# Optimization experiments

Hardware: AMD Instinct MI355X
Metric: run time of the kernel (lower is better)

## Reference

```python
import jax, jax.numpy as jnp
import numpy as np

SR = 16000
FRAME = 400      # int(0.025*SR)
HOP = 160        # int(0.01*SR)
MINP, MAXP = 32, 320   # SR/500, SR/50
NFFT_FRAME = 1024      # next pow2 >= 2*FRAME-1
NFFT_FULL = 262144     # >= samples + max hnr lag (160000+200)
LN_EPS = 1e-5


def _frame(a):
    n = a.shape[0]
    nf = (n - FRAME - 1) // HOP + 1  # len(range(0, n-FRAME, HOP))
    idx = jnp.arange(nf)[:, None] * HOP + jnp.arange(FRAME)[None, :]
    return a[idx]  # [nf, FRAME]


def _autocorr(x, nfft, nlags):
    # linear autocorrelation via FFT; nfft >= len + nlags avoids circular wrap
    X = jnp.fft.rfft(x, n=nfft)
    ac = jnp.fft.irfft(X * jnp.conj(X), n=nfft)
    return ac[..., :nlags]


def _masked_mean_std(x, m):
    cnt = m.sum()
    c = jnp.maximum(cnt, 1.0)
    mean = jnp.sum(x * m) / c
    var = jnp.sum(((x - mean) ** 2) * m) / c
    return jnp.where(cnt > 0, mean, 0.0), jnp.where(cnt > 0, jnp.sqrt(var), 0.0)


def _compact(vals, mask, fill_len):
    # pack masked values to the front (stable); first k=sum(mask) entries valid
    rank = jnp.cumsum(mask) - 1
    idx = jnp.where(mask, rank, fill_len)
    return jnp.zeros(fill_len, vals.dtype).at[idx].set(vals, mode='drop')


def _prosody_single(a):
    n = a.shape[0]
    frames = _frame(a)
    nf = frames.shape[0]
    # --- energy ---
    rms = jnp.sqrt(jnp.mean(frames ** 2, axis=-1))
    e_mean, e_std = rms.mean(), rms.std()
    # --- zero-crossing rate ---
    zcr = jnp.sum(jnp.abs(jnp.diff(jnp.sign(frames), axis=-1)), axis=-1) / (2.0 * FRAME)
    z_mean, z_std = zcr.mean(), zcr.std()
    # --- F0 via per-frame autocorrelation peak picking ---
    ac = _autocorr(frames, NFFT_FRAME, MAXP)            # [nf, 320]
    peak = jnp.argmax(ac[:, MINP:MAXP], axis=-1) + MINP  # first max, like np.argmax
    ac_pk = jnp.take_along_axis(ac, peak[:, None], axis=-1)[:, 0]
    f0 = SR / peak.astype(jnp.float32)
    valid = (ac_pk > 0.3 * ac[:, 0]) & (f0 > 50.0) & (f0 < 500.0)
    f0_mean, f0_std = _masked_mean_std(f0, valid.astype(jnp.float32))
    # --- jitter: rising threshold crossings over the whole waveform ---
    thr = 0.3 * jnp.max(jnp.abs(a))
    cross = (a[:-1] < thr) & (a[1:] >= thr)  # crossing at index i in [1, n)
    pos = jnp.arange(1, n)
    k = cross.sum()
    posarr = _compact(pos, cross, n)
    periods = (posarr[1:] - posarr[:-1]).astype(jnp.float32)
    nper = k - 1
    pmask = jnp.arange(n - 1) < nper
    mean_period = jnp.sum(periods * pmask) / jnp.maximum(nper, 1)
    pdiffs = jnp.abs(periods[1:] - periods[:-1])
    dmask = jnp.arange(n - 2) < (nper - 1)
    mean_pdiff = jnp.sum(pdiffs * dmask) / jnp.maximum(nper - 1, 1)
    jitter = jnp.where((nper >= 2) & (mean_period > 0),
                       jnp.clip(mean_pdiff / jnp.maximum(mean_period, 1e-12), 0.0, 1.0), 0.0)
    jitter = jnp.where((f0_mean < 50.0) | (f0_mean > 500.0), 0.0, jitter)
    # --- shimmer: diffs of consecutive retained (>0.01) frame peak amps ---
    amp = jnp.max(jnp.abs(frames), axis=-1)
    amask = amp > 0.01
    ka = amask.sum()
    amparr = _compact(amp, amask, nf)
    adiffs = jnp.abs(amparr[1:] - amparr[:-1])
    admask = jnp.arange(nf - 1) < (ka - 1)
    mean_amp = jnp.sum(amparr * (jnp.arange(nf) < ka)) / jnp.maximum(ka, 1)
    mean_adiff = jnp.sum(adiffs * admask) / jnp.maximum(ka - 1, 1)
    shimmer = jnp.where((ka >= 2) & (mean_amp > 0),
                        jnp.clip(mean_adiff / jnp.maximum(mean_amp, 1e-12), 0.0, 1.0), 0.0)
    # --- HNR: full-signal autocorrelation, lags 50..199 ---
    seg = _autocorr(a, NFFT_FULL, 200)[50:200]
    sig_peak = jnp.max(seg)
    noise_floor = jnp.percentile(seg, 10.0)  # numpy-default linear interpolation
    hnr = jnp.where(noise_floor > 0,
                    jnp.clip(sig_peak / jnp.maximum(noise_floor, 1e-30) / 100.0, 0.0, 1.0), 0.0)
    # --- voicing rate (energy + zcr thresholds; source truncated, see notes) ---
    voiced = (rms > 0.01) & (zcr < 0.3)
    voicing_rate = voiced.mean()
    feats = jnp.stack([f0_mean / 500.0, f0_std / 100.0, e_mean, e_std,
                       z_mean, z_std, jitter, shimmer, hnr, voicing_rate])
    metrics = jnp.stack([f0_mean, f0_std, e_mean, e_std, z_mean, z_std,
                         jitter, shimmer, hnr, voicing_rate])
    return feats, metrics


def _project(feats, W1, b1, gamma, beta, W2, b2):
    h = feats @ W1.T + b1
    mu = h.mean(-1, keepdims=True)
    var = h.var(-1, keepdims=True)
    h = (h - mu) / jnp.sqrt(var + LN_EPS) * gamma + beta
    h = jax.nn.relu(h)          # dropout = identity (eval mode)
    return h @ W2.T + b2


def setup_inputs() -> dict:
    key = jax.random.key(0)
    ks = jax.random.split(key, 7)
    B, N = 128, 160000
    return {
        'raw_audio': jax.random.normal(ks[0], (B, N), dtype=jnp.float32) * 0.5,
        'W1': jax.random.normal(ks[1], (64, 10), dtype=jnp.float32) * 0.3,
        'b1': jax.random.normal(ks[2], (64,), dtype=jnp.float32) * 0.01,
        'gamma': jnp.ones((64,), dtype=jnp.float32),
        'beta': jnp.zeros((64,), dtype=jnp.float32),
        'W2': jax.random.normal(ks[3], (128, 64), dtype=jnp.float32) * 0.1,
        'b2': jax.random.normal(ks[4], (128,), dtype=jnp.float32) * 0.01,
    }


def reference(raw_audio, W1, b1, gamma, beta, W2, b2):
    feats, metrics = jax.vmap(_prosody_single)(raw_audio)  # [B,10], [B,10]
    feats = jax.lax.stop_gradient(feats)  # torch detaches via numpy round-trip
    proj = _project(feats, W1, b1, gamma, beta, W2, b2)    # [B,128]
    return proj, metrics
```

## Files before the change

kernel.cpp:

```cpp
#include <hip/hip_runtime.h>
#include <stdint.h>

typedef unsigned int uint;
typedef unsigned short ushort;
typedef unsigned long long ull;
typedef __attribute__((ext_vector_type(8))) short bf16x8;
typedef __attribute__((ext_vector_type(4))) float f32x4;

#define SR_F 16000.0f
#define NSAMP 160000
#define NB 128
#define FRAME 400
#define HOP 160
#define NF 998
#define NHNR_CHUNK 10
#define JCH 125
#define HNR_LAGS 150
#define TJ 25
#define HWIN (32*TJ + 304)
#define NJB 10
#define TAIL0 ((NF - 1) * HOP + FRAME)

#define HXO 562
#define HREG 1116

#define OFF_RMS 0
#define OFF_ZCR (OFF_RMS + NB*NF)
#define OFF_AMP (OFF_ZCR + NB*NF)
#define OFF_F0  (OFF_AMP + NB*NF)
#define OFF_VAL (OFF_F0  + NB*NF)
#define OFF_HNR (OFF_VAL + NB*NF)
#define OFF_JST (OFF_HNR + NB*NHNR_CHUNK*HNR_LAGS)

__device__ __forceinline__ int imax_(int a, int b) { return a > b ? a : b; }
__device__ __forceinline__ int imin2_(int a, int b) { return a < b ? a : b; }

__device__ __forceinline__ int   f2i(float v) { return __builtin_bit_cast(int, v); }
__device__ __forceinline__ float i2f(int v)   { return __builtin_bit_cast(float, v); }
__device__ __forceinline__ uint  f2u(float v) { return __builtin_bit_cast(uint, v); }

#if __has_builtin(__builtin_amdgcn_permlane16_swap) && __has_builtin(__builtin_amdgcn_permlane32_swap)
#define HAVE_PLSWAP 1
#endif

template<int C>
__device__ __forceinline__ int dpp_i(int x) {
    return __builtin_amdgcn_update_dpp(0, x, C, 0xf, 0xf, true);
}
template<int C>
__device__ __forceinline__ float dpp_f(float x) { return i2f(dpp_i<C>(f2i(x))); }

__device__ __forceinline__ float wred_sum(float x) {
#ifdef HAVE_PLSWAP
    x += dpp_f<0xB1>(x);
    x += dpp_f<0x4E>(x);
    x += dpp_f<0x141>(x);
    x += dpp_f<0x140>(x);
    {
        auto r = __builtin_amdgcn_permlane16_swap(f2i(x), f2i(x), false, false);
        x = i2f((int)r[0]) + i2f((int)r[1]);
    }
    {
        auto r = __builtin_amdgcn_permlane32_swap(f2i(x), f2i(x), false, false);
        x = i2f((int)r[0]) + i2f((int)r[1]);
    }
#else
    #pragma unroll
    for (int off = 32; off; off >>= 1) x += __shfl_xor(x, off);
#endif
    return x;
}

__device__ __forceinline__ float wred_max(float x) {
#ifdef HAVE_PLSWAP
    x = fmaxf(x, dpp_f<0xB1>(x));
    x = fmaxf(x, dpp_f<0x4E>(x));
    x = fmaxf(x, dpp_f<0x141>(x));
    x = fmaxf(x, dpp_f<0x140>(x));
    {
        auto r = __builtin_amdgcn_permlane16_swap(f2i(x), f2i(x), false, false);
        x = fmaxf(i2f((int)r[0]), i2f((int)r[1]));
    }
    {
        auto r = __builtin_amdgcn_permlane32_swap(f2i(x), f2i(x), false, false);
        x = fmaxf(i2f((int)r[0]), i2f((int)r[1]));
    }
#else
    #pragma unroll
    for (int off = 32; off; off >>= 1) x = fmaxf(x, __shfl_xor(x, off));
#endif
    return x;
}

__device__ __forceinline__ int wred_imin(int x) {
#ifdef HAVE_PLSWAP
    x = imin2_(x, dpp_i<0xB1>(x));
    x = imin2_(x, dpp_i<0x4E>(x));
    x = imin2_(x, dpp_i<0x141>(x));
    x = imin2_(x, dpp_i<0x140>(x));
    {
        auto r = __builtin_amdgcn_permlane16_swap(x, x, false, false);
        x = imin2_((int)r[0], (int)r[1]);
    }
    {
        auto r = __builtin_amdgcn_permlane32_swap(x, x, false, false);
        x = imin2_((int)r[0], (int)r[1]);
    }
#else
    #pragma unroll
    for (int off = 32; off; off >>= 1) x = imin2_(x, __shfl_xor(x, off));
#endif
    return x;
}

__device__ __forceinline__ uint cvtpk_bf16(float a, float b) {
    uint r;
    asm("v_cvt_pk_bf16_f32 %0, %1, %2" : "=v"(r) : "v"(a), "v"(b));
    return r;
}

__device__ __forceinline__ bf16x8 ld_b_frag(const uint* p) {
    union { uint u[4]; bf16x8 v; } t;
    t.u[0] = p[0]; t.u[1] = p[1]; t.u[2] = p[2]; t.u[3] = p[3];
    return t.v;
}

__device__ __forceinline__ int sx_(float a, float b) {
    return (int)((f2u(a) ^ f2u(b)) >> 31);
}

struct JSt { int cnt, p0, p1, pl, pl2; float sum; };

__device__ __forceinline__ void jmerge(JSt& A, const JSt& r) {
    if (r.cnt == 0) return;
    if (A.cnt == 0) { A = r; return; }
    int pb = r.p0 - A.pl;
    A.sum += r.sum;
    if (A.cnt >= 2) A.sum += fabsf((float)(pb - (A.pl - A.pl2)));
    if (r.cnt >= 2) A.sum += fabsf((float)((r.p1 - r.p0) - pb));
    if (A.cnt == 1) A.p1 = r.p0;
    A.pl2 = (r.cnt >= 2) ? r.pl2 : A.pl;
    A.pl = r.pl;
    A.cnt += r.cnt;
}

__device__ __forceinline__ JSt jword(unsigned long long word, int wb) {
    JSt st; st.cnt = 0; st.p0 = 0; st.p1 = 0; st.pl = 0; st.pl2 = 0; st.sum = 0.f;
    while (word) {
        int b = __builtin_ctzll(word);
        word &= word - 1;
        int pos = wb + b + 1;
        if (st.cnt >= 2) st.sum += fabsf((float)((pos - st.pl) - (st.pl - st.pl2)));
        if (st.cnt == 0) st.p0 = pos;
        if (st.cnt == 1) st.p1 = pos;
        st.pl2 = st.pl; st.pl = pos; ++st.cnt;
    }
    return st;
}

__global__ __launch_bounds__(256) void k_frame(const float* __restrict__ audio,
                                               float* __restrict__ ws)
{
    __shared__ __align__(16) uint lds[4][744];
    const int tid = threadIdx.x;
    const int widx = tid >> 6, lane = tid & 63;
    const int lo = lane & 15, q = lane >> 4;
    const int s = blockIdx.y;
    const int fbase = blockIdx.x * 16 + widx * 4;
    const float* as = audio + (size_t)s * NSAMP;

    uint* base = lds[widx];
    ull* zb = (ull*)base;
    const ushort* xw_us = (const ushort*)base;

    for (int i = lane; i < 168; i += 64) {
        int zi;
        if (i < 60)       zi = i;
        else if (i < 84)  zi = 160 + (i - 60);
        else if (i < 144) zi = 185 + (i - 84);
        else              zi = 345 + (i - 144);
        zb[zi] = 0ull;
    }

    float4 tA, tB; float bnA, bnB;
    {
        int f0 = fbase; if (f0 > NF - 1) f0 = NF - 1;
        const float* a = as + (size_t)f0 * HOP;
        tA  = ((const float4*)a)[lane];
        bnA = a[4 * lane + 4];
        tB.x = tB.y = tB.z = tB.w = 0.f; bnB = 0.f;
        if (lane < 36) {
            tB  = ((const float4*)a)[64 + lane];
            bnB = (lane < 35) ? a[4 * (64 + lane) + 4] : 0.f;
        }
    }

    for (int p = 0; p < 4; ++p) {
        int f = fbase + p; if (f > NF - 1) f = NF - 1;

        float amp; int zci;
        {
            amp = fmaxf(fmaxf(fabsf(tA.x), fabsf(tA.y)),
                        fmaxf(fabsf(tA.z), fabsf(tA.w)));
            zci = sx_(tA.x, tA.y) + sx_(tA.y, tA.z)
                + sx_(tA.z, tA.w) + sx_(tA.w, bnA);
            ull w = (ull)cvtpk_bf16(tA.x, tA.y) | ((ull)cvtpk_bf16(tA.z, tA.w) << 32);
            ull o = (ull)cvtpk_bf16(tA.y, tA.z) | ((ull)cvtpk_bf16(tA.w, bnA) << 32);
            zb[60 + lane]  = w;
            zb[245 + lane] = o;
        }
        if (lane < 36) {
            amp = fmaxf(amp, fmaxf(fmaxf(fabsf(tB.x), fabsf(tB.y)),
                                   fmaxf(fabsf(tB.z), fabsf(tB.w))));
            zci += sx_(tB.x, tB.y) + sx_(tB.y, tB.z) + sx_(tB.z, tB.w);
            if (lane < 35) zci += sx_(tB.w, bnB);
            ull w = (ull)cvtpk_bf16(tB.x, tB.y) | ((ull)cvtpk_bf16(tB.z, tB.w) << 32);
            ull o = (ull)cvtpk_bf16(tB.y, tB.z) | ((ull)cvtpk_bf16(tB.w, bnB) << 32);
            zb[124 + lane] = w;
            zb[309 + lane] = o;
        }
        float zcs = wred_sum((float)zci);
        amp = wred_max(amp);

        __syncthreads();

        float4 nA, nB; float nbA = 0.f, nbB = 0.f;
        nA.x = nA.y = nA.z = nA.w = 0.f; nB = nA;
        if (p < 3) {
            int fn = fbase + p + 1; if (fn > NF - 1) fn = NF - 1;
            const float* an = as + (size_t)fn * HOP;
            nA  = ((const float4*)an)[lane];
            nbA = an[4 * lane + 4];
            if (lane < 36) {
                nB  = ((const float4*)an)[64 + lane];
                nbB = (lane < 35) ? an[4 * (64 + lane) + 4] : 0.f;
            }
        }

        f32x4 acc1 = {0.f, 0.f, 0.f, 0.f};
        f32x4 acc2 = {0.f, 0.f, 0.f, 0.f};
        const int a_eb = 240 + 8 * q - 16 * lo;
        const uint* bp = base + ((lo & 1) ? 370 : 0) + 120 + 4 * q + (lo >> 1);
        bf16x8 ah[5];

        #pragma unroll
        for (int j = 0; j < 13; ++j) {
            bf16x8 a1 = *(const bf16x8*)(xw_us + a_eb + 32 * j);
            bf16x8 b  = ld_b_frag(bp + 16 * j);
            acc1 = __builtin_amdgcn_mfma_f32_16x16x32_bf16(a1, b, acc1, 0, 0, 0);
            if (j < 5) ah[j] = a1;
            if (j >= 8)
                acc2 = __builtin_amdgcn_mfma_f32_16x16x32_bf16(ah[j - 8], b, acc2, 0, 0, 0);
        }

        float ac0 = i2f(__builtin_amdgcn_readfirstlane(f2i(acc1[0])));

        float bv = -1e30f; int bl = 1 << 30;
        #pragma unroll
        for (int r = 0; r < 4; ++r) {
            int lag = 64 * q + 16 * r + lo;
            float v = acc1[r];
            if (lag >= 32 && v > bv) { bv = v; bl = lag; }
        }
        if (q == 0) {
            #pragma unroll
            for (int r = 0; r < 4; ++r) {
                int lag = 256 + 16 * r + lo;
                float v = acc2[r];
                if (v > bv) { bv = v; bl = lag; }
            }
        }
        float mv = wred_max(bv);
        int   ml = wred_imin((bv == mv) ? bl : (1 << 30));

        if (lane == 0) {
            float f0v = SR_F / (float)ml;
            int valid = (mv > 0.3f * ac0) && (f0v > 50.f) && (f0v < 500.f);
            size_t idx = (size_t)s * NF + f;
            ws[OFF_RMS + idx] = sqrtf(fmaxf(ac0, 0.f) / (float)FRAME);
            ws[OFF_ZCR + idx] = zcs / 400.f;
            ws[OFF_AMP + idx] = amp;
            ws[OFF_F0  + idx] = f0v;
            ws[OFF_VAL + idx] = valid ? 1.f : 0.f;
        }

        tA = nA; tB = nB; bnA = nbA; bnB = nbB;
        __syncthreads();
    }
}

__global__ __launch_bounds__(256) void k_hnr(const float* __restrict__ audio,
                                             float* __restrict__ ws)
{
    __shared__ __align__(16) uint hxd[4][HREG];
    __shared__ unsigned long long msk[250];
    __shared__ __align__(16) uint pool[1504];
    __shared__ JSt sg[25];
    __shared__ float swmax[4];
    const int tid = threadIdx.x;
    const int widx = tid >> 6, lane = tid & 63;
    const int lo = lane & 15, q = lane >> 4;
    const int s = blockIdx.y;
    const int c = blockIdx.x * 4 + widx;
    const float* a = audio + (size_t)s * NSAMP;

    float (*hred)[152] = (float (*)[152])pool;
    JSt* sw = (JSt*)pool;

    uint* xwd = hxd[widx];
    uint* xod = hxd[widx] + HXO;
    const ushort* xw = (const ushort*)xwd;

    const int aoff = 240 + 8 * q - 16 * lo;
    const uint* bw = (lo & 1) ? xod : xwd;
    const int boff = 144 + 4 * q + (lo >> 1);

    f32x4 acc = {0.f, 0.f, 0.f, 0.f};

    for (int tile = 0; tile < JCH / TJ; ++tile) {
        const int g0 = 32 * (c * JCH + tile * TJ) - 288;
        for (int v = lane; v < HWIN / 4; v += 64) {
            int g = g0 + 4 * v;
            float x0, x1, x2, x3, x4;
            if (g >= 0 && g + 4 < NSAMP) {
                float4 t = *(const float4*)(a + g);
                x0 = t.x; x1 = t.y; x2 = t.z; x3 = t.w;
                x4 = a[g + 4];
            } else {
                x0 = (g     >= 0 && g     < NSAMP) ? a[g]     : 0.f;
                x1 = (g + 1 >= 0 && g + 1 < NSAMP) ? a[g + 1] : 0.f;
                x2 = (g + 2 >= 0 && g + 2 < NSAMP) ? a[g + 2] : 0.f;
                x3 = (g + 3 >= 0 && g + 3 < NSAMP) ? a[g + 3] : 0.f;
                x4 = (g + 4 >= 0 && g + 4 < NSAMP) ? a[g + 4] : 0.f;
            }
            int d = 2 * v;
            xwd[d] = cvtpk_bf16(x0, x1); xwd[d + 1] = cvtpk_bf16(x2, x3);
            xod[d] = cvtpk_bf16(x1, x2); xod[d + 1] = cvtpk_bf16(x3, x4);
        }
        asm volatile("" ::: "memory");
        __builtin_amdgcn_sched_barrier(0);

        #pragma unroll
        for (int jl = 0; jl < TJ; ++jl) {
            bf16x8 af = *(const bf16x8*)(xw + aoff + 32 * jl);
            bf16x8 bf = ld_b_frag(bw + boff + 16 * jl);
            acc = __builtin_amdgcn_mfma_f32_16x16x32_bf16(af, bf, acc, 0, 0, 0);
        }
        asm volatile("" ::: "memory");
        __builtin_amdgcn_sched_barrier(0);
    }

    #pragma unroll
    for (int r = 0; r < 4; ++r) {
        int row = 4 * q + r;
        int lag = 48 + 16 * row + lo;
        if (row < 10 && lag >= 50 && lag < 200)
            hred[widx][lag - 50] = acc[r];
    }
    __syncthreads();
    if (tid < HNR_LAGS) {
        float v = hred[0][tid] + hred[1][tid] + hred[2][tid] + hred[3][tid];
        ws[OFF_HNR + ((size_t)s * NHNR_CHUNK + blockIdx.x) * HNR_LAGS + tid] = v;
    }

    float m = 0.f;
    const float* ampA = ws + OFF_AMP + (size_t)s * NF;
    for (int i = tid; i < NF; i += 256) m = fmaxf(m, ampA[i]);
    if (tid < NSAMP - TAIL0) m = fmaxf(m, fabsf(a[TAIL0 + tid]));
    m = wred_max(m);
    if ((tid & 63) == 0) swmax[tid >> 6] = m;
    __syncthreads();
    const float thr = 0.3f * fmaxf(fmaxf(swmax[0], swmax[1]),
                                   fmaxf(swmax[2], swmax[3]));

    const int cbase = blockIdx.x * 16000;
    for (int ot = 0; ot < 9; ++ot) {
        float va[7], vb[7];
        #pragma unroll
        for (int k = 0; k < 7; ++k) {
            int off = (ot * 7 + k) * 256 + tid;
            int i = cbase + off;
            bool in = (off < 16000) && (i < NSAMP - 1);
            va[k] = in ? a[i] : 1e30f;
            vb[k] = in ? a[i + 1] : 1e30f;
        }
        #pragma unroll
        for (int k = 0; k < 7; ++k) {
            int off = (ot * 7 + k) * 256 + tid;
            bool fl = (va[k] < thr) && (vb[k] >= thr);
            unsigned long long bal = __ballot(fl);
            int w = off >> 6;
            if ((tid & 63) == 0 && w < 250) msk[w] = bal;
        }
    }
    __syncthreads();

    if (tid < 250) sw[tid] = jword(msk[tid], cbase + tid * 64);
    __syncthreads();
    if (tid < 25) {
        JSt A = sw[10 * tid];
        #pragma unroll
        for (int k = 1; k < 10; ++k) jmerge(A, sw[10 * tid + k]);
        sg[tid] = A;
    }
    __syncthreads();
    if (tid == 0) {
        JSt A = sg[0];
        for (int k = 1; k < 25; ++k) jmerge(A, sg[k]);
        float* jp = ws + OFF_JST + ((size_t)s * NJB + blockIdx.x) * 6;
        jp[0] = (float)A.cnt; jp[1] = (float)A.p0; jp[2] = (float)A.p1;
        jp[3] = (float)A.pl;  jp[4] = (float)A.pl2; jp[5] = A.sum;
    }
}

__global__ __launch_bounds__(256) void k_final(const float* __restrict__ ws,
        const float* __restrict__ W1, const float* __restrict__ b1,
        const float* __restrict__ gam, const float* __restrict__ bet,
        const float* __restrict__ W2, const float* __restrict__ b2,
        float* __restrict__ out)
{
    __shared__ float samp[NF];
    __shared__ float sac[HNR_LAGS];
    __shared__ float sred[32];
    __shared__ float sstat[11];
    __shared__ float sjit[4];
    __shared__ float sfeats[10];
    __shared__ float shid[64];
    __shared__ float ssa[250][5];
    __shared__ float ssg[25][5];

    const int s = blockIdx.x;
    const int tid = threadIdx.x;
    const float* rmsA = ws + OFF_RMS + (size_t)s * NF;
    const float* zcrA = ws + OFF_ZCR + (size_t)s * NF;
    const float* ampA = ws + OFF_AMP + (size_t)s * NF;
    const float* f0A  = ws + OFF_F0  + (size_t)s * NF;
    const float* valA = ws + OFF_VAL + (size_t)s * NF;

    float a0=0,a1=0,a2=0,a3=0,a4=0,a5=0,a6=0,a7=0;
    for (int i = tid; i < NF; i += 256) {
        float r = rmsA[i], z = zcrA[i], f0 = f0A[i], v = valA[i];
        samp[i] = ampA[i];
        a0 += r; a1 += r * r; a2 += z; a3 += z * z;
        a4 += f0 * v; a5 += f0 * f0 * v; a6 += v;
        a7 += (r > 0.01f && z < 0.3f) ? 1.f : 0.f;
    }
    #pragma unroll
    for (int off = 32; off; off >>= 1) {
        a0 += __shfl_xor(a0, off); a1 += __shfl_xor(a1, off);
        a2 += __shfl_xor(a2, off); a3 += __shfl_xor(a3, off);
        a4 += __shfl_xor(a4, off); a5 += __shfl_xor(a5, off);
        a6 += __shfl_xor(a6, off); a7 += __shfl_xor(a7, off);
    }
    if ((tid & 63) == 0) {
        int w = tid >> 6;
        sred[w*8+0]=a0; sred[w*8+1]=a1; sred[w*8+2]=a2; sred[w*8+3]=a3;
        sred[w*8+4]=a4; sred[w*8+5]=a5; sred[w*8+6]=a6; sred[w*8+7]=a7;
    }
    __syncthreads();

    if (tid < HNR_LAGS) {
        float acc = 0.f;
        const float* p = ws + OFF_HNR + (size_t)s * NHNR_CHUNK * HNR_LAGS + tid;
        #pragma unroll
        for (int c = 0; c < NHNR_CHUNK; ++c) acc += p[c * HNR_LAGS];
        sac[tid] = acc;
    }
    if (tid == 0) {
        for (int k = 0; k < 8; ++k)
            sstat[k] = sred[k] + sred[8+k] + sred[16+k] + sred[24+k];
    }
    if (tid < 250) {
        int i0 = tid * 4;
        float cnt=0.f, first=0.f, last=0.f, ssum=0.f, sad=0.f;
        #pragma unroll
        for (int k = 0; k < 4; ++k) {
            int i = i0 + k;
            if (i < NF) {
                float av = samp[i];
                if (av > 0.01f) {
                    if (cnt >= 1.f) sad += fabsf(av - last);
                    else first = av;
                    ssum += av; last = av; cnt += 1.f;
                }
            }
        }
        ssa[tid][0]=cnt; ssa[tid][1]=first; ssa[tid][2]=last;
        ssa[tid][3]=ssum; ssa[tid][4]=sad;
    }
    __syncthreads();

    if (tid < HNR_LAGS) {
        float v = sac[tid];
        int r = 0;
        for (int j = 0; j < HNR_LAGS; ++j) {
            float vj = sac[j];
            r += (vj < v) || (vj == v && j < tid);
        }
        if (r == 14) sstat[8] = v;
        if (r == 15) sstat[9] = v;
    }
    if (tid == 160) {
        const float* jp = ws + OFF_JST + (size_t)s * NJB * 6;
        JSt A; A.cnt = 0; A.p0 = 0; A.p1 = 0; A.pl = 0; A.pl2 = 0; A.sum = 0.f;
        for (int c = 0; c < NJB; ++c) {
            JSt r;
            r.cnt = (int)jp[c*6+0]; r.p0 = (int)jp[c*6+1]; r.p1 = (int)jp[c*6+2];
            r.pl  = (int)jp[c*6+3]; r.pl2 = (int)jp[c*6+4]; r.sum = jp[c*6+5];
            jmerge(A, r);
        }
        sjit[0] = (float)A.cnt; sjit[1] = (float)A.p0;
        sjit[2] = (float)A.pl;  sjit[3] = A.sum;
    }
    if (tid == 192) {
        float mx = sac[0];
        for (int j = 1; j < HNR_LAGS; ++j) mx = fmaxf(mx, sac[j]);
        sstat[10] = mx;
    }
    if (tid >= 200 && tid < 225) {
        int t2 = tid - 200;
        float cnt=0.f, first=0.f, last=0.f, ssum=0.f, sad=0.f;
        #pragma unroll
        for (int k = 0; k < 10; ++k) {
            int j = 10 * t2 + k;
            float c2 = ssa[j][0];
            if (c2 > 0.f) {
                if (cnt > 0.f) sad += ssa[j][4] + fabsf(ssa[j][1] - last);
                else { first = ssa[j][1]; sad += ssa[j][4]; }
                ssum += ssa[j][3]; last = ssa[j][2]; cnt += c2;
            }
        }
        ssg[t2][0]=cnt; ssg[t2][1]=first; ssg[t2][2]=last;
        ssg[t2][3]=ssum; ssg[t2][4]=sad;
    }
    __syncthreads();

    if (tid == 0) {
        float S_r = sstat[0], S_r2 = sstat[1], S_z = sstat[2], S_z2 = sstat[3];
        float S_f = sstat[4], S_f2 = sstat[5], S_v = sstat[6], S_voi = sstat[7];
        float e_mean = S_r / (float)NF;
        float e_std  = sqrtf(fmaxf(S_r2 / (float)NF - e_mean * e_mean, 0.f));
        float z_mean = S_z / (float)NF;
        float z_std  = sqrtf(fmaxf(S_z2 / (float)NF - z_mean * z_mean, 0.f));
        float f0_mean = 0.f, f0_std = 0.f;
        if (S_v > 0.f) {
            f0_mean = S_f / S_v;
            f0_std  = sqrtf(fmaxf(S_f2 / S_v - f0_mean * f0_mean, 0.f));
        }
        int k = (int)sjit[0];
        float pp0 = sjit[1], ppl = sjit[2], psum = sjit[3];
        int nper = k - 1;
        float mean_period = (k >= 2) ? (ppl - pp0) / (float)(k - 1) : 0.f;
        float mean_pd = psum / (float)imax_(nper - 1, 1);
        float jit = (nper >= 2 && mean_period > 0.f)
            ? fminf(fmaxf(mean_pd / fmaxf(mean_period, 1e-12f), 0.f), 1.f) : 0.f;
        if (f0_mean < 50.f || f0_mean > 500.f) jit = 0.f;
        float noise = 0.1f * sstat[8] + 0.9f * sstat[9];
        float hnr = (noise > 0.f)
            ? fminf(fmaxf(sstat[10] / fmaxf(noise, 1e-30f) / 100.f, 0.f), 1.f) : 0.f;

        float cnt=0.f, first=0.f, last=0.f, ssum=0.f, sad=0.f;
        for (int c = 0; c < 25; ++c) {
            float c2 = ssg[c][0];
            if (c2 > 0.f) {
                if (cnt > 0.f) sad += ssg[c][4] + fabsf(ssg[c][1] - last);
                else { first = ssg[c][1]; sad += ssg[c][4]; }
                ssum += ssg[c][3]; last = ssg[c][2]; cnt += c2;
            }
        }
        int ka = (int)cnt;
        float mean_amp = ssum / (float)imax_(ka, 1);
        float mean_ad  = sad  / (float)imax_(ka - 1, 1);
        float shim = (ka >= 2 && mean_amp > 0.f)
            ? fminf(fmaxf(mean_ad / fmaxf(mean_amp, 1e-12f), 0.f), 1.f) : 0.f;
        float voice = S_voi / (float)NF;

        float mt[10] = {f0_mean, f0_std, e_mean, e_std, z_mean, z_std, jit, shim, hnr, voice};
        for (int i = 0; i < 10; ++i) out[NB * 128 + s * 10 + i] = mt[i];
        sfeats[0] = f0_mean / 500.f;
        sfeats[1] = f0_std / 100.f;
        for (int i = 2; i < 10; ++i) sfeats[i] = mt[i];
    }
    __syncthreads();

    if (tid < 64) {
        float h = b1[tid];
        #pragma unroll
        for (int i = 0; i < 10; ++i) h = fmaf(sfeats[i], W1[tid * 10 + i], h);
        float sum = h, sq = h * h;
        #pragma unroll
        for (int off = 32; off; off >>= 1) {
            sum += __shfl_xor(sum, off);
            sq  += __shfl_xor(sq, off);
        }
        float mu = sum / 64.f;
        float var = sq / 64.f - mu * mu;
        float hn = (h - mu) * rsqrtf(var + 1e-5f) * gam[tid] + bet[tid];
        shid[tid] = fmaxf(hn, 0.f);
    }
    __syncthreads();
    if (tid < 128) {
        float accv = b2[tid];
        #pragma unroll 8
        for (int j = 0; j < 64; ++j) accv = fmaf(shid[j], W2[tid * 64 + j], accv);
        out[(size_t)s * 128 + tid] = accv;
    }
}

extern "C" void kernel_launch(void* const* d_in, const int* in_sizes, int n_in,
                              void* d_out, int out_size, void* d_ws, size_t ws_size,
                              hipStream_t stream)
{
    const float* audio = (const float*)d_in[0];
    const float* W1    = (const float*)d_in[1];
    const float* b1    = (const float*)d_in[2];
    const float* gam   = (const float*)d_in[3];
    const float* bet   = (const float*)d_in[4];
    const float* W2    = (const float*)d_in[5];
    const float* b2    = (const float*)d_in[6];
    float* out = (float*)d_out;
    float* ws  = (float*)d_ws;

    hipLaunchKernelGGL(k_frame, dim3((NF + 15) / 16, NB), dim3(256), 0, stream, audio, ws);
    hipLaunchKernelGGL(k_hnr,   dim3(NJB, NB),            dim3(256), 0, stream, audio, ws);
    hipLaunchKernelGGL(k_final, dim3(NB),                 dim3(256), 0, stream,
                       ws, W1, b1, gam, bet, W2, b2, out);
}
```

Baseline: 231.2 us.

## Fuse final reduction kernel into HNR kernel via last-block atomic counter

Removes the separate k_final launch. Each k_hnr block increments a per-sample atomic counter after writing its partial results, and the last block for each sample performs the final feature reduction and projection, reusing the shared-memory buffers already allocated. k_frame resets the counter at the start of each call. This saves a kernel launch and the gap between kernels, at the cost of threadfences, an atomic per block, and a serialized tail on the last-arriving blocks.

```diff
diff --git a/kernel.cpp b/kernel.cpp
--- a/kernel.cpp
+++ b/kernel.cpp
@@ -31,6 +31,7 @@
 #define OFF_VAL (OFF_F0  + NB*NF)
 #define OFF_HNR (OFF_VAL + NB*NF)
 #define OFF_JST (OFF_HNR + NB*NHNR_CHUNK*HNR_LAGS)
+#define OFF_CNT (OFF_JST + NB*NJB*6)
 
 __device__ __forceinline__ int imax_(int a, int b) { return a > b ? a : b; }
 __device__ __forceinline__ int imin2_(int a, int b) { return a < b ? a : b; }
@@ -169,6 +170,9 @@
     const int fbase = blockIdx.x * 16 + widx * 4;
     const float* as = audio + (size_t)s * NSAMP;
 
+    if (blockIdx.x == 0 && tid == 0)
+        ((uint*)(ws + OFF_CNT))[s] = 0u;
+
     uint* base = lds[widx];
     ull* zb = (ull*)base;
     const ushort* xw_us = (const ushort*)base;
@@ -290,13 +294,18 @@
 }
 
 __global__ __launch_bounds__(256) void k_hnr(const float* __restrict__ audio,
-                                             float* __restrict__ ws)
+        float* __restrict__ ws,
+        const float* __restrict__ W1, const float* __restrict__ b1,
+        const float* __restrict__ gam, const float* __restrict__ bet,
+        const float* __restrict__ W2, const float* __restrict__ b2,
+        float* __restrict__ out)
 {
     __shared__ __align__(16) uint hxd[4][HREG];
     __shared__ unsigned long long msk[250];
     __shared__ __align__(16) uint pool[1504];
     __shared__ JSt sg[25];
     __shared__ float swmax[4];
+    __shared__ uint s_last;
     const int tid = threadIdx.x;
     const int widx = tid >> 6, lane = tid & 63;
     const int lo = lane & 15, q = lane >> 4;
@@ -411,31 +420,35 @@
         jp[0] = (float)A.cnt; jp[1] = (float)A.p0; jp[2] = (float)A.p1;
         jp[3] = (float)A.pl;  jp[4] = (float)A.pl2; jp[5] = A.sum;
     }
-}
-
-__global__ __launch_bounds__(256) void k_final(const float* __restrict__ ws,
-        const float* __restrict__ W1, const float* __restrict__ b1,
-        const float* __restrict__ gam, const float* __restrict__ bet,
-        const float* __restrict__ W2, const float* __restrict__ b2,
-        float* __restrict__ out)
-{
-    __shared__ float samp[NF];
-    __shared__ float sac[HNR_LAGS];
-    __shared__ float sred[32];
-    __shared__ float sstat[11];
-    __shared__ float sjit[4];
-    __shared__ float sfeats[10];
-    __shared__ float shid[64];
-    __shared__ float ssa[250][5];
-    __shared__ float ssg[25][5];
-
-    const int s = blockIdx.x;
-    const int tid = threadIdx.x;
+
+    __syncthreads();
+    if (tid == 0) {
+        __threadfence();
+        uint old = atomicAdd((uint*)(ws + OFF_CNT) + s, 1u);
+        s_last = (old == NJB - 1) ? 1u : 0u;
+    }
+    __syncthreads();
+    if (!s_last) return;
+    __threadfence();
+
+    float* fsh    = (float*)&hxd[0][0];
+    float* samp   = fsh;
+    float* sac    = fsh + 1000;
+    float* sredf  = fsh + 1152;
+    float* sstat  = fsh + 1184;
+    float* sjit   = fsh + 1196;
+    float* sfeats = fsh + 1200;
+    float* shid   = fsh + 1216;
+    float* sjst   = fsh + 1280;
+    float (*ssa)[5] = (float (*)[5])pool;
+    float (*ssg)[5] = (float (*)[5])msk;
+
     const float* rmsA = ws + OFF_RMS + (size_t)s * NF;
     const float* zcrA = ws + OFF_ZCR + (size_t)s * NF;
-    const float* ampA = ws + OFF_AMP + (size_t)s * NF;
     const float* f0A  = ws + OFF_F0  + (size_t)s * NF;
     const float* valA = ws + OFF_VAL + (size_t)s * NF;
+
+    __syncthreads();
 
     float a0=0,a1=0,a2=0,a3=0,a4=0,a5=0,a6=0,a7=0;
     for (int i = tid; i < NF; i += 256) {
@@ -445,6 +458,7 @@
         a4 += f0 * v; a5 += f0 * f0 * v; a6 += v;
         a7 += (r > 0.01f && z < 0.3f) ? 1.f : 0.f;
     }
+    if (tid < NJB * 6) sjst[tid] = ws[OFF_JST + (size_t)s * NJB * 6 + tid];
     #pragma unroll
     for (int off = 32; off; off >>= 1) {
         a0 += __shfl_xor(a0, off); a1 += __shfl_xor(a1, off);
@@ -454,21 +468,21 @@
     }
     if ((tid & 63) == 0) {
         int w = tid >> 6;
-        sred[w*8+0]=a0; sred[w*8+1]=a1; sred[w*8+2]=a2; sred[w*8+3]=a3;
-        sred[w*8+4]=a4; sred[w*8+5]=a5; sred[w*8+6]=a6; sred[w*8+7]=a7;
+        sredf[w*8+0]=a0; sredf[w*8+1]=a1; sredf[w*8+2]=a2; sredf[w*8+3]=a3;
+        sredf[w*8+4]=a4; sredf[w*8+5]=a5; sredf[w*8+6]=a6; sredf[w*8+7]=a7;
     }
     __syncthreads();
 
     if (tid < HNR_LAGS) {
-        float acc = 0.f;
+        float accv = 0.f;
         const float* p = ws + OFF_HNR + (size_t)s * NHNR_CHUNK * HNR_LAGS + tid;
         #pragma unroll
-        for (int c = 0; c < NHNR_CHUNK; ++c) acc += p[c * HNR_LAGS];
-        sac[tid] = acc;
+        for (int cc = 0; cc < NHNR_CHUNK; ++cc) accv += p[cc * HNR_LAGS];
+        sac[tid] = accv;
     }
     if (tid == 0) {
         for (int k = 0; k < 8; ++k)
-            sstat[k] = sred[k] + sred[8+k] + sred[16+k] + sred[24+k];
+            sstat[k] = sredf[k] + sredf[8+k] + sredf[16+k] + sredf[24+k];
     }
     if (tid < 250) {
         int i0 = tid * 4;
@@ -501,12 +515,12 @@
         if (r == 15) sstat[9] = v;
     }
     if (tid == 160) {
-        const float* jp = ws + OFF_JST + (size_t)s * NJB * 6;
         JSt A; A.cnt = 0; A.p0 = 0; A.p1 = 0; A.pl = 0; A.pl2 = 0; A.sum = 0.f;
-        for (int c = 0; c < NJB; ++c) {
+        for (int cc = 0; cc < NJB; ++cc) {
             JSt r;
-            r.cnt = (int)jp[c*6+0]; r.p0 = (int)jp[c*6+1]; r.p1 = (int)jp[c*6+2];
-            r.pl  = (int)jp[c*6+3]; r.pl2 = (int)jp[c*6+4]; r.sum = jp[c*6+5];
+            r.cnt = (int)sjst[cc*6+0]; r.p0 = (int)sjst[cc*6+1];
+            r.p1  = (int)sjst[cc*6+2]; r.pl = (int)sjst[cc*6+3];
+            r.pl2 = (int)sjst[cc*6+4]; r.sum = sjst[cc*6+5];
             jmerge(A, r);
         }
         sjit[0] = (float)A.cnt; sjit[1] = (float)A.p0;
@@ -560,12 +574,12 @@
             ? fminf(fmaxf(sstat[10] / fmaxf(noise, 1e-30f) / 100.f, 0.f), 1.f) : 0.f;
 
         float cnt=0.f, first=0.f, last=0.f, ssum=0.f, sad=0.f;
-        for (int c = 0; c < 25; ++c) {
-            float c2 = ssg[c][0];
+        for (int cc = 0; cc < 25; ++cc) {
+            float c2 = ssg[cc][0];
             if (c2 > 0.f) {
-                if (cnt > 0.f) sad += ssg[c][4] + fabsf(ssg[c][1] - last);
-                else { first = ssg[c][1]; sad += ssg[c][4]; }
-                ssum += ssg[c][3]; last = ssg[c][2]; cnt += c2;
+                if (cnt > 0.f) sad += ssg[cc][4] + fabsf(ssg[cc][1] - last);
+                else { first = ssg[cc][1]; sad += ssg[cc][4]; }
+                ssum += ssg[cc][3]; last = ssg[cc][2]; cnt += c2;
             }
         }
         int ka = (int)cnt;
@@ -622,7 +636,6 @@
     float* ws  = (float*)d_ws;
 
     hipLaunchKernelGGL(k_frame, dim3((NF + 15) / 16, NB), dim3(256), 0, stream, audio, ws);
-    hipLaunchKernelGGL(k_hnr,   dim3(NJB, NB),            dim3(256), 0, stream, audio, ws);
-    hipLaunchKernelGGL(k_final, dim3(NB),                 dim3(256), 0, stream,
-                       ws, W1, b1, gam, bet, W2, b2, out);
-}
+    hipLaunchKernelGGL(k_hnr,   dim3(NJB, NB),            dim3(256), 0, stream,
+                       audio, ws, W1, b1, gam, bet, W2, b2, out);
+}
```

Measured after the change: 286.7 us. 24.0% more time.
